# Performance work log

Measured on AMD Instinct MI355X. Metric: run time of the kernel, lower is better.

## Reference

```python
import jax, jax.numpy as jnp
import numpy as np

B, N, E = 8, 50000, 400000
DIMS = [4, 64, 64, 3]
K = 3
EPS = 1e-5
NEG_SLOPE = 0.01


def _gcn_norm(edge_index, num_nodes):
    # TAGConv uses gcn_norm with unit edge weights and add_self_loops=False.
    row, col = edge_index[0], edge_index[1]
    w = jnp.ones(row.shape[0], dtype=jnp.float32)
    deg = jax.ops.segment_sum(w, col, num_segments=num_nodes)  # in-degree at target
    dis = jnp.where(deg > 0, jnp.power(jnp.maximum(deg, 1.0), -0.5), 0.0)
    return dis[row] * dis[col]  # [E]


def _tag_conv(x, W, b, row, col, norm, num_nodes):
    # x: [B, N, Fin]; W: [K+1, Fin, Fout]; b: [Fout]
    out = jnp.einsum('bnf,fg->bng', x, W[0])
    h = x
    for k in range(1, W.shape[0]):
        msg = h[:, row, :] * norm[None, :, None]            # [B, E, Fin] gather
        h = jnp.zeros((x.shape[0], num_nodes, x.shape[2]), x.dtype).at[:, col, :].add(msg)  # scatter-add
        out = out + jnp.einsum('bnf,fg->bng', h, W[k])
    return out + b


def _batchnorm(x2d, gamma, beta):
    # training-mode BatchNorm1d over batch dim (biased variance, eps=1e-5)
    mean = jnp.mean(x2d, axis=0)
    var = jnp.mean(jnp.square(x2d - mean), axis=0)
    return gamma * (x2d - mean) * jax.lax.rsqrt(var + EPS) + beta


def _leaky_relu(x):
    return jnp.where(x >= 0, x, NEG_SLOPE * x)


def setup_inputs() -> dict:
    key = jax.random.key(0)
    ks = jax.random.split(key, 12)
    inp = {}
    inp['x'] = jax.random.normal(ks[0], (B, N, DIMS[0]), dtype=jnp.float32)
    inp['edge_index'] = jax.random.randint(ks[1], (2, E), 0, N, dtype=jnp.int64)
    inp['val_min'] = jax.random.uniform(ks[2], (N, 3), dtype=jnp.float32) - 1.5
    inp['val_max'] = jax.random.uniform(ks[3], (N, 3), dtype=jnp.float32) + 0.5
    for l in range(3):
        fin, fout = DIMS[l], DIMS[l + 1]
        scale = 1.0 / np.sqrt(fin)
        inp[f'W{l}'] = jax.random.uniform(ks[4 + l], (K + 1, fin, fout), minval=-scale, maxval=scale, dtype=jnp.float32)
        inp[f'b{l}'] = jnp.zeros((fout,), jnp.float32)
    for l in range(2):
        inp[f'gamma{l}'] = jnp.ones((N * DIMS[l + 1],), jnp.float32)
        inp[f'beta{l}'] = jnp.zeros((N * DIMS[l + 1],), jnp.float32)
    return inp


def reference(x, edge_index, val_min, val_max, W0, b0, W1, b1, W2, b2,
              gamma0, beta0, gamma1, beta1):
    row, col = edge_index[0], edge_index[1]
    norm = _gcn_norm(edge_index, N)
    Ws = [W0, W1, W2]
    bs = [b0, b1, b2]
    gammas = [gamma0, gamma1]
    betas = [beta0, beta1]
    out = x
    for layer in range(2):  # num_layers - 1 hidden layers
        out = _tag_conv(out, Ws[layer], bs[layer], row, col, norm, N)
        d = DIMS[layer + 1]
        out = _batchnorm(out.reshape(-1, N * d), gammas[layer], betas[layer]).reshape(-1, N, d)
        out = _leaky_relu(out)
    out = _tag_conv(out, Ws[2], bs[2], row, col, norm, N)  # [B, N, 3]
    # non_linearity: gamma = min + (max - min) / (1 + exp(U))
    return val_min[None] + (val_max - val_min)[None] / (1.0 + jnp.exp(out))
```

## Files before the change

kernel.cpp:

```cpp
#include <hip/hip_runtime.h>
#include <math.h>

constexpr int B = 8;
constexpr int N = 50000;
constexpr int E = 400000;
constexpr float BN_EPS = 1e-5f;
constexpr float NEG = 0.01f;


__device__ __forceinline__ unsigned clamp_src(int s) {
    unsigned u = (unsigned)s;
    return (u < (unsigned)N) ? u : 0u;
}

__device__ __forceinline__ unsigned pack_bf16(float a, float b) {
    unsigned ua = __float_as_uint(a);
    unsigned ub = __float_as_uint(b);
    ua = (ua + 0x7FFFu + ((ua >> 16) & 1u)) >> 16;
    ub = (ub + 0x7FFFu + ((ub >> 16) & 1u)) >> 16;
    return (ub << 16) | (ua & 0xFFFFu);
}
__device__ __forceinline__ float unpack_lo(unsigned u) { return __uint_as_float(u << 16); }
__device__ __forceinline__ float unpack_hi(unsigned u) { return __uint_as_float(u & 0xFFFF0000u); }

__device__ __forceinline__ void store_row64_bf(uint4* p, const float acc[64]) {
#pragma unroll
    for (int q = 0; q < 8; ++q) {
        uint4 v;
        v.x = pack_bf16(acc[q * 8 + 0], acc[q * 8 + 1]);
        v.y = pack_bf16(acc[q * 8 + 2], acc[q * 8 + 3]);
        v.z = pack_bf16(acc[q * 8 + 4], acc[q * 8 + 5]);
        v.w = pack_bf16(acc[q * 8 + 6], acc[q * 8 + 7]);
        p[q] = v;
    }
}


__global__ __launch_bounds__(256) void deg_kernel(const int* __restrict__ col, float* __restrict__ deg) {
    int e = blockIdx.x * blockDim.x + threadIdx.x;
    if (e < E) atomicAdd(&deg[clamp_src(col[e])], 1.0f);
}

__global__ __launch_bounds__(256) void scan1_kernel(const float* __restrict__ deg,
                                                    int* __restrict__ part, int* __restrict__ bsum) {
    __shared__ int sm[4];
    int i = blockIdx.x * blockDim.x + threadIdx.x;
    int v = (i < N) ? (int)deg[i] : 0;
    int lane = threadIdx.x & 63, wv = threadIdx.x >> 6;
    int x = v;
#pragma unroll
    for (int off = 1; off < 64; off <<= 1) {
        int t = __shfl_up(x, off);
        if (lane >= off) x += t;
    }
    if (lane == 63) sm[wv] = x;
    __syncthreads();
    int add = 0;
#pragma unroll
    for (int w = 0; w < 4; ++w) if (w < wv) add += sm[w];
    if (i < N) part[i] = x - v + add;
    if (threadIdx.x == blockDim.x - 1) bsum[blockIdx.x] = x + add;
}

__global__ __launch_bounds__(256) void scan2_kernel(const int* __restrict__ bsum, int* __restrict__ boff,
                                                    int nb, int* __restrict__ rowptr) {
    __shared__ int sm[4];
    int i = threadIdx.x;
    int v = (i < nb) ? bsum[i] : 0;
    int lane = i & 63, wv = i >> 6;
    int x = v;
#pragma unroll
    for (int off = 1; off < 64; off <<= 1) {
        int t = __shfl_up(x, off);
        if (lane >= off) x += t;
    }
    if (lane == 63) sm[wv] = x;
    __syncthreads();
    int add = 0;
#pragma unroll
    for (int w = 0; w < 4; ++w) if (w < wv) add += sm[w];
    if (i < nb) boff[i] = x - v + add;
    if (i == 0) rowptr[N] = E;
}

__global__ __launch_bounds__(256) void scan3_kernel(const int* __restrict__ part, const int* __restrict__ boff,
                                                    int* __restrict__ rowptr) {
    int i = blockIdx.x * blockDim.x + threadIdx.x;
    if (i < N) rowptr[i] = part[i] + boff[blockIdx.x];
}

__global__ __launch_bounds__(256) void fill_kernel(const int* __restrict__ row, const int* __restrict__ col,
                                                   const int* __restrict__ rowptr,
                                                   int* __restrict__ cursor, int* __restrict__ csr_src) {
    int e = blockIdx.x * blockDim.x + threadIdx.x;
    if (e >= E) return;
    unsigned r = clamp_src(row[e]), c = clamp_src(col[e]);
    unsigned p = (unsigned)(rowptr[c] + atomicAdd(&cursor[c], 1));
    if (p >= (unsigned)E) p = E - 1;
    csr_src[p] = (int)r;
}

__global__ __launch_bounds__(256) void dis_kernel(float* __restrict__ deg) {
    int i = blockIdx.x * blockDim.x + threadIdx.x;
    if (i < N) {
        float d = deg[i];
        deg[i] = (d > 0.f) ? rsqrtf(d) : 0.f;
    }
}


template<bool INBF>
__global__ __launch_bounds__(256) void xprop_kernel(const void* __restrict__ xin, const int* __restrict__ rowptr,
                                                    const int* __restrict__ csr_src, const float* __restrict__ dis,
                                                    uint2* __restrict__ xout) {
    int b = blockIdx.x & 7;
    int n = (blockIdx.x >> 3) * blockDim.x + threadIdx.x;
    if (n >= N) return;
    float a0 = 0.f, a1 = 0.f, a2 = 0.f, a3 = 0.f;
    int beg = rowptr[n], end = rowptr[n + 1];
    if (beg < 0) beg = 0;
    if (end > E) end = E;
    for (int i = beg; i < end; ++i) {
        unsigned s = clamp_src(csr_src[i]);
        float w = dis[s];
        if constexpr (!INBF) {
            float4 v = *((const float4*)xin + (size_t)b * N + s);
            a0 = fmaf(w, v.x, a0); a1 = fmaf(w, v.y, a1);
            a2 = fmaf(w, v.z, a2); a3 = fmaf(w, v.w, a3);
        } else {
            uint2 v = *((const uint2*)xin + (size_t)b * N + s);
            a0 = fmaf(w, unpack_lo(v.x), a0); a1 = fmaf(w, unpack_hi(v.x), a1);
            a2 = fmaf(w, unpack_lo(v.y), a2); a3 = fmaf(w, unpack_hi(v.y), a3);
        }
    }
    float dn = dis[n];
    uint2 o;
    o.x = pack_bf16(a0 * dn, a1 * dn);
    o.y = pack_bf16(a2 * dn, a3 * dn);
    xout[(size_t)b * N + n] = o;
}


__device__ __forceinline__ void load_xv(const float4* __restrict__ x0, const uint2* __restrict__ x1,
                                        const uint2* __restrict__ x2, const uint2* __restrict__ x3,
                                        size_t ro, float xv[16]) {
    float4 v = x0[ro];
    xv[0] = v.x; xv[1] = v.y; xv[2] = v.z; xv[3] = v.w;
    uint2 u1 = x1[ro], u2 = x2[ro], u3 = x3[ro];
    xv[4] = unpack_lo(u1.x); xv[5] = unpack_hi(u1.x); xv[6] = unpack_lo(u1.y); xv[7] = unpack_hi(u1.y);
    xv[8] = unpack_lo(u2.x); xv[9] = unpack_hi(u2.x); xv[10] = unpack_lo(u2.y); xv[11] = unpack_hi(u2.y);
    xv[12] = unpack_lo(u3.x); xv[13] = unpack_hi(u3.x); xv[14] = unpack_lo(u3.y); xv[15] = unpack_hi(u3.y);
}


__global__ __launch_bounds__(256) void build_h1_kernel(const float4* __restrict__ x0, const uint2* __restrict__ x1,
                                                       const uint2* __restrict__ x2, const uint2* __restrict__ x3,
                                                       const float* __restrict__ W0,
                                                       const float* __restrict__ gamma, const float* __restrict__ beta,
                                                       uint4* __restrict__ h1) {
    int gid = blockIdx.x * blockDim.x + threadIdx.x;
    int node = gid >> 6;
    int lane = gid & 63;
    int fg = lane >> 3, b = lane & 7;
    if (node >= N) return;
    size_t ro = (size_t)b * N + node;
    float xv[16];
    load_xv(x0, x1, x2, x3, ro, xv);
    float z[8];
#pragma unroll
    for (int j = 0; j < 8; ++j) z[j] = 0.f;
#pragma unroll
    for (int kf = 0; kf < 16; ++kf) {
        const float* wr = W0 + kf * 64 + fg * 8;
        float4 wa = *(const float4*)wr;
        float4 wb = *(const float4*)(wr + 4);
        float xs = xv[kf];
        z[0] = fmaf(xs, wa.x, z[0]); z[1] = fmaf(xs, wa.y, z[1]);
        z[2] = fmaf(xs, wa.z, z[2]); z[3] = fmaf(xs, wa.w, z[3]);
        z[4] = fmaf(xs, wb.x, z[4]); z[5] = fmaf(xs, wb.y, z[5]);
        z[6] = fmaf(xs, wb.z, z[6]); z[7] = fmaf(xs, wb.w, z[7]);
    }
    const float* gp = gamma + (size_t)node * 64 + fg * 8;
    const float* bp = beta + (size_t)node * 64 + fg * 8;
    float h[8];
#pragma unroll
    for (int j = 0; j < 8; ++j) {
        float v = z[j];
        float s = v, s2 = v * v;
        s += __shfl_xor(s, 1);  s += __shfl_xor(s, 2);  s += __shfl_xor(s, 4);
        s2 += __shfl_xor(s2, 1); s2 += __shfl_xor(s2, 2); s2 += __shfl_xor(s2, 4);
        float mean = s * 0.125f;
        float var = fmaf(-mean, mean, s2 * 0.125f);
        float rs = rsqrtf(var + BN_EPS);
        float o = fmaf(gp[j] * rs, v - mean, bp[j]);
        h[j] = (o >= 0.f) ? o : NEG * o;
    }
    uint4 o;
    o.x = pack_bf16(h[0], h[1]);
    o.y = pack_bf16(h[2], h[3]);
    o.z = pack_bf16(h[4], h[5]);
    o.w = pack_bf16(h[6], h[7]);
    h1[ro * 8 + fg] = o;
}


__device__ __forceinline__ void fma_row(float acc[64], float w, const uint4 r[8]) {
#pragma unroll
    for (int q = 0; q < 8; ++q) {
        uint4 v = r[q];
        acc[q * 8 + 0] = fmaf(w, unpack_lo(v.x), acc[q * 8 + 0]);
        acc[q * 8 + 1] = fmaf(w, unpack_hi(v.x), acc[q * 8 + 1]);
        acc[q * 8 + 2] = fmaf(w, unpack_lo(v.y), acc[q * 8 + 2]);
        acc[q * 8 + 3] = fmaf(w, unpack_hi(v.y), acc[q * 8 + 3]);
        acc[q * 8 + 4] = fmaf(w, unpack_lo(v.z), acc[q * 8 + 4]);
        acc[q * 8 + 5] = fmaf(w, unpack_hi(v.z), acc[q * 8 + 5]);
        acc[q * 8 + 6] = fmaf(w, unpack_lo(v.w), acc[q * 8 + 6]);
        acc[q * 8 + 7] = fmaf(w, unpack_hi(v.w), acc[q * 8 + 7]);
    }
}

__device__ __forceinline__ void gather64_bf(const uint4* __restrict__ ub8, int beg, int end,
                                            const int* __restrict__ csr_src, const float* __restrict__ dis,
                                            float acc[64]) {
    if (beg < 0) beg = 0;
    if (end > E) end = E;
    int i = beg;
    for (; i + 1 < end; i += 2) {
        unsigned s0 = clamp_src(csr_src[i]);
        unsigned s1 = clamp_src(csr_src[i + 1]);
        float w0 = dis[s0], w1 = dis[s1];
        const uint4* p0 = ub8 + (size_t)s0 * 8;
        const uint4* p1 = ub8 + (size_t)s1 * 8;
        uint4 r0[8], r1[8];
#pragma unroll
        for (int q = 0; q < 8; ++q) r0[q] = p0[q];
#pragma unroll
        for (int q = 0; q < 8; ++q) r1[q] = p1[q];
        fma_row(acc, w0, r0);
        fma_row(acc, w1, r1);
    }
    if (i < end) {
        unsigned s0 = clamp_src(csr_src[i]);
        float w0 = dis[s0];
        const uint4* p0 = ub8 + (size_t)s0 * 8;
        uint4 r0[8];
#pragma unroll
        for (int q = 0; q < 8; ++q) r0[q] = p0[q];
        fma_row(acc, w0, r0);
    }
}

__device__ __forceinline__ void dense64_bf(const uint4* __restrict__ hp8, const float* __restrict__ W, float acc[64]) {
#pragma unroll 1
    for (int kk = 0; kk < 4; ++kk) {
        float hreg[16];
        uint4 va = hp8[kk * 2], vb = hp8[kk * 2 + 1];
        hreg[0] = unpack_lo(va.x); hreg[1] = unpack_hi(va.x);
        hreg[2] = unpack_lo(va.y); hreg[3] = unpack_hi(va.y);
        hreg[4] = unpack_lo(va.z); hreg[5] = unpack_hi(va.z);
        hreg[6] = unpack_lo(va.w); hreg[7] = unpack_hi(va.w);
        hreg[8] = unpack_lo(vb.x); hreg[9] = unpack_hi(vb.x);
        hreg[10] = unpack_lo(vb.y); hreg[11] = unpack_hi(vb.y);
        hreg[12] = unpack_lo(vb.z); hreg[13] = unpack_hi(vb.z);
        hreg[14] = unpack_lo(vb.w); hreg[15] = unpack_hi(vb.w);
        const float* Wp = W + kk * 16 * 64;
#pragma unroll
        for (int k = 0; k < 16; ++k) {
            float hv = hreg[k];
#pragma unroll
            for (int c = 0; c < 64; ++c)
                acc[c] = fmaf(hv, Wp[k * 64 + c], acc[c]);
        }
    }
}


template<int MODE>
__global__ __launch_bounds__(256) void hopM_kernel(const uint4* __restrict__ u_in, const int* __restrict__ rowptr,
                                                   const int* __restrict__ csr_src, const float* __restrict__ dis,
                                                   const uint4* __restrict__ h1, int b0, int bmask, int bshift,
                                                   const float* __restrict__ Wk, const float* __restrict__ bias,
                                                   uint4* __restrict__ u_out) {
    int bl = blockIdx.x & bmask;
    int n = (blockIdx.x >> bshift) * blockDim.x + threadIdx.x;
    if (n >= N) return;
    float acc[64];
#pragma unroll
    for (int f = 0; f < 64; ++f) acc[f] = 0.f;
    if constexpr (MODE > 0) {
        gather64_bf(u_in + (size_t)bl * N * 8, rowptr[n], rowptr[n + 1], csr_src, dis, acc);
        float dn = dis[n];
#pragma unroll
        for (int f = 0; f < 64; ++f) acc[f] *= dn;
    }
    if constexpr (MODE == 2) {
#pragma unroll
        for (int f = 0; f < 64; ++f) acc[f] += bias[f];
    }
    dense64_bf(h1 + ((size_t)(b0 + bl) * N + n) * 8, Wk, acc);
    store_row64_bf(u_out + ((size_t)bl * N + n) * 8, acc);
}


__global__ __launch_bounds__(256) void bn_project_kernel(const uint4* __restrict__ zlo, const uint4* __restrict__ zhi,
                                                         const float* __restrict__ gamma, const float* __restrict__ beta,
                                                         const float* __restrict__ W2, float* __restrict__ y) {
    int gid = blockIdx.x * blockDim.x + threadIdx.x;
    int node = gid >> 6;
    int lane = gid & 63;
    int fg = lane >> 3, b = lane & 7;
    if (node >= N) return;
    const uint4* zp = (b < 4) ? (zlo + ((size_t)b * N + node) * 8)
                              : (zhi + ((size_t)(b - 4) * N + node) * 8);
    uint4 v = zp[fg];
    float h[8] = {unpack_lo(v.x), unpack_hi(v.x), unpack_lo(v.y), unpack_hi(v.y),
                  unpack_lo(v.z), unpack_hi(v.z), unpack_lo(v.w), unpack_hi(v.w)};
    const float* gp = gamma + (size_t)node * 64 + fg * 8;
    const float* bp = beta + (size_t)node * 64 + fg * 8;
#pragma unroll
    for (int j = 0; j < 8; ++j) {
        float val = h[j];
        float s = val, s2 = val * val;
        s += __shfl_xor(s, 1);  s += __shfl_xor(s, 2);  s += __shfl_xor(s, 4);
        s2 += __shfl_xor(s2, 1); s2 += __shfl_xor(s2, 2); s2 += __shfl_xor(s2, 4);
        float mean = s * 0.125f;
        float var = fmaf(-mean, mean, s2 * 0.125f);
        float rs = rsqrtf(var + BN_EPS);
        float o = fmaf(gp[j] * rs, val - mean, bp[j]);
        h[j] = (o >= 0.f) ? o : NEG * o;
    }
    float p[12];
#pragma unroll
    for (int k = 0; k < 4; ++k) {
#pragma unroll
        for (int c = 0; c < 3; ++c) {
            float s = 0.f;
#pragma unroll
            for (int j = 0; j < 8; ++j)
                s = fmaf(h[j], W2[k * 192 + (fg * 8 + j) * 3 + c], s);
            p[k * 3 + c] = s;
        }
    }
#pragma unroll
    for (int t = 8; t < 64; t <<= 1) {
#pragma unroll
        for (int i = 0; i < 12; ++i)
            p[i] += __shfl_xor(p[i], t);
    }
    if (fg == 0) {
        size_t bn3 = ((size_t)b * N + node) * 3;
#pragma unroll
        for (int k = 0; k < 4; ++k)
#pragma unroll
            for (int c = 0; c < 3; ++c)
                y[(size_t)k * B * N * 3 + bn3 + c] = p[k * 3 + c];
    }
}


__global__ __launch_bounds__(256) void qprop_kernel(const float* __restrict__ vin, const int* __restrict__ rowptr,
                                                    const int* __restrict__ csr_src, const float* __restrict__ dis,
                                                    const float* __restrict__ add, float* __restrict__ vout) {
    int b = blockIdx.x & 7;
    int n = (blockIdx.x >> 3) * blockDim.x + threadIdx.x;
    if (n >= N) return;
    float a0 = 0.f, a1 = 0.f, a2 = 0.f;
    int beg = rowptr[n], end = rowptr[n + 1];
    if (beg < 0) beg = 0;
    if (end > E) end = E;
    const float* base = vin + (size_t)b * N * 3;
    for (int i = beg; i < end; ++i) {
        unsigned s = clamp_src(csr_src[i]);
        float w = dis[s];
        const float* p = base + (size_t)s * 3;
        a0 = fmaf(w, p[0], a0);
        a1 = fmaf(w, p[1], a1);
        a2 = fmaf(w, p[2], a2);
    }
    float dn = dis[n];
    const float* ap = add + ((size_t)b * N + n) * 3;
    float* op = vout + ((size_t)b * N + n) * 3;
    op[0] = fmaf(a0, dn, ap[0]);
    op[1] = fmaf(a1, dn, ap[1]);
    op[2] = fmaf(a2, dn, ap[2]);
}

__global__ __launch_bounds__(256) void qfinal_kernel(const float* __restrict__ vin, const int* __restrict__ rowptr,
                                                     const int* __restrict__ csr_src, const float* __restrict__ dis,
                                                     const float* __restrict__ y0, const float* __restrict__ b2,
                                                     const float* __restrict__ vmin, const float* __restrict__ vmax,
                                                     float* __restrict__ out) {
    int b = blockIdx.x & 7;
    int n = (blockIdx.x >> 3) * blockDim.x + threadIdx.x;
    if (n >= N) return;
    float a0 = 0.f, a1 = 0.f, a2 = 0.f;
    int beg = rowptr[n], end = rowptr[n + 1];
    if (beg < 0) beg = 0;
    if (end > E) end = E;
    const float* base = vin + (size_t)b * N * 3;
    for (int i = beg; i < end; ++i) {
        unsigned s = clamp_src(csr_src[i]);
        float w = dis[s];
        const float* p = base + (size_t)s * 3;
        a0 = fmaf(w, p[0], a0);
        a1 = fmaf(w, p[1], a1);
        a2 = fmaf(w, p[2], a2);
    }
    float dn = dis[n];
    size_t bn3 = ((size_t)b * N + n) * 3;
    const float* yp = y0 + bn3;
    float g0 = fmaf(a0, dn, yp[0]) + b2[0];
    float g1 = fmaf(a1, dn, yp[1]) + b2[1];
    float g2 = fmaf(a2, dn, yp[2]) + b2[2];
    float mn0 = vmin[n * 3 + 0], mx0 = vmax[n * 3 + 0];
    float mn1 = vmin[n * 3 + 1], mx1 = vmax[n * 3 + 1];
    float mn2 = vmin[n * 3 + 2], mx2 = vmax[n * 3 + 2];
    float* op = out + bn3;
    op[0] = mn0 + (mx0 - mn0) / (1.f + expf(g0));
    op[1] = mn1 + (mx1 - mn1) / (1.f + expf(g1));
    op[2] = mn2 + (mx2 - mn2) / (1.f + expf(g2));
}


extern "C" void kernel_launch(void* const* d_in, const int* in_sizes, int n_in,
                              void* d_out, int out_size, void* d_ws, size_t ws_size,
                              hipStream_t stream) {
    const float* x      = (const float*)d_in[0];
    const int*   ei     = (const int*)d_in[1];
    const int*   rowi   = ei;
    const int*   coli   = ei + E;
    const float* vmin   = (const float*)d_in[2];
    const float* vmax   = (const float*)d_in[3];
    const float* W0     = (const float*)d_in[4];
    const float* W1     = (const float*)d_in[6];
    const float* b1v    = (const float*)d_in[7];
    const float* W2     = (const float*)d_in[8];
    const float* b2v    = (const float*)d_in[9];
    const float* gamma0 = (const float*)d_in[10];
    const float* beta0  = (const float*)d_in[11];
    const float* gamma1 = (const float*)d_in[12];
    const float* beta1  = (const float*)d_in[13];
    float* out = (float*)d_out;

    const size_t BN3  = (size_t)B * N * 3;
    const size_t H1FL = (size_t)B * N * 32;
    const size_t UCFL = (size_t)4 * N * 32;
    const size_t XBFL = (size_t)B * N * 2;

    auto rnd = [](size_t nf) { return (nf + 63) & ~(size_t)63; };
    size_t off = 0;
    auto alloc = [&](size_t nfloats) -> float* {
        float* p = (float*)d_ws + off;
        off += rnd(nfloats);
        return p;
    };
    float* deg     = alloc(N);
    int*   rowptr  = (int*)alloc(N + 1);
    int*   part    = (int*)alloc(N);
    int*   bsum    = (int*)alloc(256);
    int*   boff    = (int*)alloc(256);
    int*   cursor  = (int*)alloc(N);
    int*   csr_src = (int*)alloc(E);
    float* h1      = alloc(H1FL);

    const size_t avail_fl = ws_size / 4;
    const size_t need_full = off + 2 * H1FL + 4096;
    bool full = (avail_fl >= need_full);

    float *uA, *uB, *uC = nullptr;
    if (full) {
        uA = alloc(H1FL);
        uB = alloc(H1FL);
    } else {
        uA = alloc(UCFL);
        uB = alloc(UCFL);
        uC = alloc(UCFL);
    }
    uint2* xb1 = (uint2*)uA;
    uint2* xb2 = (uint2*)((float*)uA + XBFL);
    uint2* xb3 = (uint2*)((float*)uA + 2 * XBFL);
    float* y   = h1;
    float* v_a = h1 + rnd(4 * BN3);
    float* v_b = v_a + rnd(BN3);

    const int GE  = (E + 255) / 256;
    const int GN  = (N + 255) / 256;
    const int GB8 = GN * 8;
    const int GH4 = GN * 4;
    const int GW  = (N * 64) / 256;
    dim3 blk(256);

    hipMemsetAsync(deg, 0, N * sizeof(float), stream);
    hipMemsetAsync(cursor, 0, N * sizeof(int), stream);
    deg_kernel<<<GE, blk, 0, stream>>>(coli, deg);
    scan1_kernel<<<GN, blk, 0, stream>>>(deg, part, bsum);
    scan2_kernel<<<1, blk, 0, stream>>>(bsum, boff, GN, rowptr);
    scan3_kernel<<<GN, blk, 0, stream>>>(part, boff, rowptr);
    fill_kernel<<<GE, blk, 0, stream>>>(rowi, coli, rowptr, cursor, csr_src);
    dis_kernel<<<GN, blk, 0, stream>>>(deg);
    const float* dis = deg;

    xprop_kernel<false><<<GB8, blk, 0, stream>>>(x,   rowptr, csr_src, dis, xb1);
    xprop_kernel<true><<<GB8, blk, 0, stream>>>(xb1, rowptr, csr_src, dis, xb2);
    xprop_kernel<true><<<GB8, blk, 0, stream>>>(xb2, rowptr, csr_src, dis, xb3);
    build_h1_kernel<<<GW, blk, 0, stream>>>((const float4*)x, xb1, xb2, xb3, W0, gamma0, beta0, (uint4*)h1);

    const uint4* H1 = (const uint4*)h1;
    if (full) {
        hopM_kernel<0><<<GB8, blk, 0, stream>>>(nullptr, rowptr, csr_src, dis, H1, 0, 7, 3,
                                                W1 + 3 * 4096, nullptr, (uint4*)uA);
        hopM_kernel<1><<<GB8, blk, 0, stream>>>((const uint4*)uA, rowptr, csr_src, dis, H1, 0, 7, 3,
                                                W1 + 2 * 4096, nullptr, (uint4*)uB);
        hopM_kernel<1><<<GB8, blk, 0, stream>>>((const uint4*)uB, rowptr, csr_src, dis, H1, 0, 7, 3,
                                                W1 + 1 * 4096, nullptr, (uint4*)uA);
        hopM_kernel<2><<<GB8, blk, 0, stream>>>((const uint4*)uA, rowptr, csr_src, dis, H1, 0, 7, 3,
                                                W1, b1v, (uint4*)uB);
        bn_project_kernel<<<GW, blk, 0, stream>>>((const uint4*)uB, (const uint4*)(uB + 4 * (size_t)N * 32),
                                                  gamma1, beta1, W2, y);
    } else {
        hopM_kernel<0><<<GB8, blk, 0, stream>>>(nullptr, rowptr, csr_src, dis, H1, 0, 7, 3,
                                                W1 + 3 * 4096, nullptr, (uint4*)uA);
        hopM_kernel<1><<<GH4, blk, 0, stream>>>((const uint4*)uA, rowptr, csr_src, dis, H1, 0, 3, 2,
                                                W1 + 2 * 4096, nullptr, (uint4*)uC);
        hopM_kernel<1><<<GH4, blk, 0, stream>>>((const uint4*)uC, rowptr, csr_src, dis, H1, 0, 3, 2,
                                                W1 + 1 * 4096, nullptr, (uint4*)uA);
        hopM_kernel<2><<<GH4, blk, 0, stream>>>((const uint4*)uA, rowptr, csr_src, dis, H1, 0, 3, 2,
                                                W1, b1v, (uint4*)uC);
        hopM_kernel<1><<<GH4, blk, 0, stream>>>((const uint4*)uB, rowptr, csr_src, dis, H1, 4, 3, 2,
                                                W1 + 2 * 4096, nullptr, (uint4*)uA);
        hopM_kernel<1><<<GH4, blk, 0, stream>>>((const uint4*)uA, rowptr, csr_src, dis, H1, 4, 3, 2,
                                                W1 + 1 * 4096, nullptr, (uint4*)uB);
        hopM_kernel<2><<<GH4, blk, 0, stream>>>((const uint4*)uB, rowptr, csr_src, dis, H1, 4, 3, 2,
                                                W1, b1v, (uint4*)uA);
        bn_project_kernel<<<GW, blk, 0, stream>>>((const uint4*)uC, (const uint4*)uA,
                                                  gamma1, beta1, W2, y);
    }

    qprop_kernel<<<GB8, blk, 0, stream>>>(y + 3 * BN3, rowptr, csr_src, dis, y + 2 * BN3, v_a);
    qprop_kernel<<<GB8, blk, 0, stream>>>(v_a, rowptr, csr_src, dis, y + 1 * BN3, v_b);
    qfinal_kernel<<<GB8, blk, 0, stream>>>(v_b, rowptr, csr_src, dis, y, b2v, vmin, vmax, out);
}
```

Measured before the change: 928.3 us.

## Sort nodes by in-degree to balance gather work in hop kernels

Builds a counting-sort permutation of nodes by in-degree (histogram, scan, rank) and has the gather-mode hop kernels process nodes in that order. Threads in a wavefront then see similar neighbor counts, which cuts divergence in the per-node gather loop. The cost is scattered, non-coalesced row accesses for h1 and the outputs, plus three small setup kernels. It also reorders the BatchNorm shuffle reductions for more instruction-level parallelism and merges the memsets into one.

New measurement: 1.283 ms. 1.38x slower.

```diff
diff --git a/kernel.cpp b/kernel.cpp
--- a/kernel.cpp
+++ b/kernel.cpp
@@ -100,12 +100,50 @@
     csr_src[p] = (int)r;
 }
 
-__global__ __launch_bounds__(256) void dis_kernel(float* __restrict__ deg) {
+
+__global__ __launch_bounds__(256) void hist_kernel(const float* __restrict__ deg, int* __restrict__ hist) {
     int i = blockIdx.x * blockDim.x + threadIdx.x;
     if (i < N) {
-        float d = deg[i];
-        deg[i] = (d > 0.f) ? rsqrtf(d) : 0.f;
-    }
+        int d = (int)deg[i];
+        if (d > 1023) d = 1023;
+        atomicAdd(&hist[d], 1);
+    }
+}
+
+__global__ __launch_bounds__(256) void hscan_kernel(const int* __restrict__ hist, int* __restrict__ binstart) {
+    __shared__ int sm[4];
+    int t = threadIdx.x;
+    int h0 = hist[t * 4 + 0], h1 = hist[t * 4 + 1], h2 = hist[t * 4 + 2], h3 = hist[t * 4 + 3];
+    int sum = h0 + h1 + h2 + h3;
+    int lane = t & 63, wv = t >> 6;
+    int x = sum;
+#pragma unroll
+    for (int off = 1; off < 64; off <<= 1) {
+        int v = __shfl_up(x, off);
+        if (lane >= off) x += v;
+    }
+    if (lane == 63) sm[wv] = x;
+    __syncthreads();
+    int add = 0;
+#pragma unroll
+    for (int w = 0; w < 4; ++w) if (w < wv) add += sm[w];
+    int excl = x - sum + add;
+    binstart[t * 4 + 0] = excl;
+    binstart[t * 4 + 1] = excl + h0;
+    binstart[t * 4 + 2] = excl + h0 + h1;
+    binstart[t * 4 + 3] = excl + h0 + h1 + h2;
+}
+
+__global__ __launch_bounds__(256) void rank_dis_kernel(float* __restrict__ deg, const int* __restrict__ binstart,
+                                                       int* __restrict__ bincur, int* __restrict__ perm) {
+    int n = blockIdx.x * blockDim.x + threadIdx.x;
+    if (n >= N) return;
+    float d = deg[n];
+    int di = (int)d;
+    if (di > 1023) di = 1023;
+    int r = binstart[di] + atomicAdd(&bincur[di], 1);
+    if ((unsigned)r < (unsigned)N) perm[r] = n;
+    deg[n] = (d > 0.f) ? rsqrtf(d) : 0.f;
 }
 
 
@@ -180,19 +218,26 @@
         z[4] = fmaf(xs, wb.x, z[4]); z[5] = fmaf(xs, wb.y, z[5]);
         z[6] = fmaf(xs, wb.z, z[6]); z[7] = fmaf(xs, wb.w, z[7]);
     }
+    float s[8], s2[8];
+#pragma unroll
+    for (int j = 0; j < 8; ++j) { s[j] = z[j]; s2[j] = z[j] * z[j]; }
+#pragma unroll
+    for (int off = 1; off < 8; off <<= 1) {
+#pragma unroll
+        for (int j = 0; j < 8; ++j) {
+            s[j] += __shfl_xor(s[j], off);
+            s2[j] += __shfl_xor(s2[j], off);
+        }
+    }
     const float* gp = gamma + (size_t)node * 64 + fg * 8;
     const float* bp = beta + (size_t)node * 64 + fg * 8;
     float h[8];
 #pragma unroll
     for (int j = 0; j < 8; ++j) {
-        float v = z[j];
-        float s = v, s2 = v * v;
-        s += __shfl_xor(s, 1);  s += __shfl_xor(s, 2);  s += __shfl_xor(s, 4);
-        s2 += __shfl_xor(s2, 1); s2 += __shfl_xor(s2, 2); s2 += __shfl_xor(s2, 4);
-        float mean = s * 0.125f;
-        float var = fmaf(-mean, mean, s2 * 0.125f);
+        float mean = s[j] * 0.125f;
+        float var = fmaf(-mean, mean, s2[j] * 0.125f);
         float rs = rsqrtf(var + BN_EPS);
-        float o = fmaf(gp[j] * rs, v - mean, bp[j]);
+        float o = fmaf(gp[j] * rs, z[j] - mean, bp[j]);
         h[j] = (o >= 0.f) ? o : NEG * o;
     }
     uint4 o;
@@ -278,12 +323,16 @@
 template<int MODE>
 __global__ __launch_bounds__(256) void hopM_kernel(const uint4* __restrict__ u_in, const int* __restrict__ rowptr,
                                                    const int* __restrict__ csr_src, const float* __restrict__ dis,
+                                                   const int* __restrict__ perm,
                                                    const uint4* __restrict__ h1, int b0, int bmask, int bshift,
                                                    const float* __restrict__ Wk, const float* __restrict__ bias,
                                                    uint4* __restrict__ u_out) {
     int bl = blockIdx.x & bmask;
-    int n = (blockIdx.x >> bshift) * blockDim.x + threadIdx.x;
-    if (n >= N) return;
+    int r = (blockIdx.x >> bshift) * blockDim.x + threadIdx.x;
+    if (r >= N) return;
+    int n;
+    if constexpr (MODE > 0) n = (int)clamp_src(perm[r]);
+    else n = r;
     float acc[64];
 #pragma unroll
     for (int f = 0; f < 64; ++f) acc[f] = 0.f;
@@ -315,18 +364,25 @@
     uint4 v = zp[fg];
     float h[8] = {unpack_lo(v.x), unpack_hi(v.x), unpack_lo(v.y), unpack_hi(v.y),
                   unpack_lo(v.z), unpack_hi(v.z), unpack_lo(v.w), unpack_hi(v.w)};
+    float s[8], s2[8];
+#pragma unroll
+    for (int j = 0; j < 8; ++j) { s[j] = h[j]; s2[j] = h[j] * h[j]; }
+#pragma unroll
+    for (int off = 1; off < 8; off <<= 1) {
+#pragma unroll
+        for (int j = 0; j < 8; ++j) {
+            s[j] += __shfl_xor(s[j], off);
+            s2[j] += __shfl_xor(s2[j], off);
+        }
+    }
     const float* gp = gamma + (size_t)node * 64 + fg * 8;
     const float* bp = beta + (size_t)node * 64 + fg * 8;
 #pragma unroll
     for (int j = 0; j < 8; ++j) {
-        float val = h[j];
-        float s = val, s2 = val * val;
-        s += __shfl_xor(s, 1);  s += __shfl_xor(s, 2);  s += __shfl_xor(s, 4);
-        s2 += __shfl_xor(s2, 1); s2 += __shfl_xor(s2, 2); s2 += __shfl_xor(s2, 4);
-        float mean = s * 0.125f;
-        float var = fmaf(-mean, mean, s2 * 0.125f);
+        float mean = s[j] * 0.125f;
+        float var = fmaf(-mean, mean, s2[j] * 0.125f);
         float rs = rsqrtf(var + BN_EPS);
-        float o = fmaf(gp[j] * rs, val - mean, bp[j]);
+        float o = fmaf(gp[j] * rs, h[j] - mean, bp[j]);
         h[j] = (o >= 0.f) ? o : NEG * o;
     }
     float p[12];
@@ -334,11 +390,11 @@
     for (int k = 0; k < 4; ++k) {
 #pragma unroll
         for (int c = 0; c < 3; ++c) {
-            float s = 0.f;
+            float sv = 0.f;
 #pragma unroll
             for (int j = 0; j < 8; ++j)
-                s = fmaf(h[j], W2[k * 192 + (fg * 8 + j) * 3 + c], s);
-            p[k * 3 + c] = s;
+                sv = fmaf(h[j], W2[k * 192 + (fg * 8 + j) * 3 + c], sv);
+            p[k * 3 + c] = sv;
         }
     }
 #pragma unroll
@@ -455,11 +511,16 @@
         return p;
     };
     float* deg     = alloc(N);
+    int*   cursor  = (int*)alloc(N);
+    int*   hist    = (int*)alloc(1024);
+    int*   bincur  = (int*)alloc(1024);
+    size_t zero_bytes = (rnd(N) * 2 + 2048) * 4;
     int*   rowptr  = (int*)alloc(N + 1);
     int*   part    = (int*)alloc(N);
     int*   bsum    = (int*)alloc(256);
     int*   boff    = (int*)alloc(256);
-    int*   cursor  = (int*)alloc(N);
+    int*   binstart= (int*)alloc(1024);
+    int*   perm    = (int*)alloc(N);
     int*   csr_src = (int*)alloc(E);
     float* h1      = alloc(H1FL);
 
@@ -490,14 +551,15 @@
     const int GW  = (N * 64) / 256;
     dim3 blk(256);
 
-    hipMemsetAsync(deg, 0, N * sizeof(float), stream);
-    hipMemsetAsync(cursor, 0, N * sizeof(int), stream);
+    hipMemsetAsync(deg, 0, zero_bytes, stream);
     deg_kernel<<<GE, blk, 0, stream>>>(coli, deg);
     scan1_kernel<<<GN, blk, 0, stream>>>(deg, part, bsum);
     scan2_kernel<<<1, blk, 0, stream>>>(bsum, boff, GN, rowptr);
     scan3_kernel<<<GN, blk, 0, stream>>>(part, boff, rowptr);
     fill_kernel<<<GE, blk, 0, stream>>>(rowi, coli, rowptr, cursor, csr_src);
-    dis_kernel<<<GN, blk, 0, stream>>>(deg);
+    hist_kernel<<<GN, blk, 0, stream>>>(deg, hist);
+    hscan_kernel<<<1, blk, 0, stream>>>(hist, binstart);
+    rank_dis_kernel<<<GN, blk, 0, stream>>>(deg, binstart, bincur, perm);
     const float* dis = deg;
 
     xprop_kernel<false><<<GB8, blk, 0, stream>>>(x,   rowptr, csr_src, dis, xb1);
@@ -507,30 +569,30 @@
 
     const uint4* H1 = (const uint4*)h1;
     if (full) {
-        hopM_kernel<0><<<GB8, blk, 0, stream>>>(nullptr, rowptr, csr_src, dis, H1, 0, 7, 3,
+        hopM_kernel<0><<<GB8, blk, 0, stream>>>(nullptr, rowptr, csr_src, dis, perm, H1, 0, 7, 3,
                                                 W1 + 3 * 4096, nullptr, (uint4*)uA);
-        hopM_kernel<1><<<GB8, blk, 0, stream>>>((const uint4*)uA, rowptr, csr_src, dis, H1, 0, 7, 3,
+        hopM_kernel<1><<<GB8, blk, 0, stream>>>((const uint4*)uA, rowptr, csr_src, dis, perm, H1, 0, 7, 3,
                                                 W1 + 2 * 4096, nullptr, (uint4*)uB);
-        hopM_kernel<1><<<GB8, blk, 0, stream>>>((const uint4*)uB, rowptr, csr_src, dis, H1, 0, 7, 3,
+        hopM_kernel<1><<<GB8, blk, 0, stream>>>((const uint4*)uB, rowptr, csr_src, dis, perm, H1, 0, 7, 3,
                                                 W1 + 1 * 4096, nullptr, (uint4*)uA);
-        hopM_kernel<2><<<GB8, blk, 0, stream>>>((const uint4*)uA, rowptr, csr_src, dis, H1, 0, 7, 3,
+        hopM_kernel<2><<<GB8, blk, 0, stream>>>((const uint4*)uA, rowptr, csr_src, dis, perm, H1, 0, 7, 3,
                                                 W1, b1v, (uint4*)uB);
         bn_project_kernel<<<GW, blk, 0, stream>>>((const uint4*)uB, (const uint4*)(uB + 4 * (size_t)N * 32),
                                                   gamma1, beta1, W2, y);
     } else {
-        hopM_kernel<0><<<GB8, blk, 0, stream>>>(nullptr, rowptr, csr_src, dis, H1, 0, 7, 3,
+        hopM_kernel<0><<<GB8, blk, 0, stream>>>(nullptr, rowptr, csr_src, dis, perm, H1, 0, 7, 3,
                                                 W1 + 3 * 4096, nullptr, (uint4*)uA);
-        hopM_kernel<1><<<GH4, blk, 0, stream>>>((const uint4*)uA, rowptr, csr_src, dis, H1, 0, 3, 2,
+        hopM_kernel<1><<<GH4, blk, 0, stream>>>((const uint4*)uA, rowptr, csr_src, dis, perm, H1, 0, 3, 2,
                                                 W1 + 2 * 4096, nullptr, (uint4*)uC);
-        hopM_kernel<1><<<GH4, blk, 0, stream>>>((const uint4*)uC, rowptr, csr_src, dis, H1, 0, 3, 2,
+        hopM_kernel<1><<<GH4, blk, 0, stream>>>((const uint4*)uC, rowptr, csr_src, dis, perm, H1, 0, 3, 2,
                                                 W1 + 1 * 4096, nullptr, (uint4*)uA);
-        hopM_kernel<2><<<GH4, blk, 0, stream>>>((const uint4*)uA, rowptr, csr_src, dis, H1, 0, 3, 2,
+        hopM_kernel<2><<<GH4, blk, 0, stream>>>((const uint4*)uA, rowptr, csr_src, dis, perm, H1, 0, 3, 2,
                                                 W1, b1v, (uint4*)uC);
-        hopM_kernel<1><<<GH4, blk, 0, stream>>>((const uint4*)uB, rowptr, csr_src, dis, H1, 4, 3, 2,
+        hopM_kernel<1><<<GH4, blk, 0, stream>>>((const uint4*)uB, rowptr, csr_src, dis, perm, H1, 4, 3, 2,
                                                 W1 + 2 * 4096, nullptr, (uint4*)uA);
-        hopM_kernel<1><<<GH4, blk, 0, stream>>>((const uint4*)uA, rowptr, csr_src, dis, H1, 4, 3, 2,
+        hopM_kernel<1><<<GH4, blk, 0, stream>>>((const uint4*)uA, rowptr, csr_src, dis, perm, H1, 4, 3, 2,
                                                 W1 + 1 * 4096, nullptr, (uint4*)uB);
-        hopM_kernel<2><<<GH4, blk, 0, stream>>>((const uint4*)uB, rowptr, csr_src, dis, H1, 4, 3, 2,
+        hopM_kernel<2><<<GH4, blk, 0, stream>>>((const uint4*)uB, rowptr, csr_src, dis, perm, H1, 4, 3, 2,
                                                 W1, b1v, (uint4*)uA);
         bn_project_kernel<<<GW, blk, 0, stream>>>((const uint4*)uC, (const uint4*)uA,
                                                   gamma1, beta1, W2, y);
```
